# Kernel optimization log

Measured on AMD Instinct MI355X. Metric: run time of the kernel, lower is better.

## Reference

```python
import jax, jax.numpy as jnp
import numpy as np

D_MODEL = 2048
D_INNER = 4096   # expand * d_model == ngroups * d_state
D_XB = 1024
N_HEADS = 32     # = ngroups
HEAD_DIM = 128   # = d_state
N_KV_HEADS = D_XB // HEAD_DIM  # 8
N_REP = N_HEADS // N_KV_HEADS  # 4
D_IN_PROJ = D_INNER + 2 * D_XB + D_INNER + N_HEADS  # 10272
ROPE_BASE = 10000.0


def setup_inputs() -> dict:
    key = jax.random.key(0)
    k1, k2, k3 = jax.random.split(key, 3)
    u = jax.random.normal(k1, (2, 2048, D_MODEL), dtype=jnp.float32)
    W_in = jax.random.normal(k2, (D_IN_PROJ, D_MODEL), dtype=jnp.float32) * (1.0 / np.sqrt(D_MODEL))
    W_out = jax.random.normal(k3, (D_MODEL, D_INNER), dtype=jnp.float32) * (1.0 / np.sqrt(D_INNER))
    return {"u": u, "W_in": W_in, "W_out": W_out}


def _rotate_half(x):
    x1, x2 = jnp.split(x, 2, axis=-1)
    return jnp.concatenate((-x2, x1), axis=-1)


def _rope_cos_sin(seqlen, dim, dtype):
    inv_freq = 1.0 / (ROPE_BASE ** (jnp.arange(0, dim, 2, dtype=jnp.float32) / dim))
    pos = jnp.arange(seqlen, dtype=jnp.float32)
    freqs = pos[:, None] * inv_freq[None, :]          # [S, dim/2]
    emb = jnp.concatenate((freqs, freqs), axis=-1)    # [S, dim]
    return jnp.cos(emb).astype(dtype), jnp.sin(emb).astype(dtype)


def reference(u, W_in, W_out):
    # NOTE: the module's forward short-circuits (early return) into a GQA
    # attention path; the SSM code after the return is dead.
    B, S, _ = u.shape
    zxbcdt = jnp.einsum('bsd,ed->bse', u, W_in)       # [B, S, D_IN_PROJ]
    # split: z (d_inner), x (d_xb), B (d_xb), C (d_inner), dt (nheads); d_mlp = 0
    o0 = D_INNER
    x = zxbcdt[..., o0:o0 + D_XB]
    Bm = zxbcdt[..., o0 + D_XB:o0 + 2 * D_XB]
    C = zxbcdt[..., o0 + 2 * D_XB:o0 + 2 * D_XB + D_INNER]
    # q = C (32 heads), k = B (8 heads), v = x (8 heads); [B, H, S, Dh]
    q = C.reshape(B, S, N_HEADS, HEAD_DIM).transpose(0, 2, 1, 3)
    k = Bm.reshape(B, S, N_KV_HEADS, HEAD_DIM).transpose(0, 2, 1, 3)
    v = x.reshape(B, S, N_KV_HEADS, HEAD_DIM).transpose(0, 2, 1, 3)
    cos, sin = _rope_cos_sin(S, HEAD_DIM, u.dtype)    # [S, Dh]
    cos = cos[None, None]                             # [1, 1, S, Dh]
    sin = sin[None, None]
    q = q * cos + _rotate_half(q) * sin
    k = k * cos + _rotate_half(k) * sin
    # repeat_kv: repeat_interleave along head dim
    k = jnp.repeat(k, N_REP, axis=1)
    v = jnp.repeat(v, N_REP, axis=1)
    scale = 1.0 / np.sqrt(HEAD_DIM)
    scores = jnp.einsum('bhqd,bhkd->bhqk', q, k) * scale
    causal = jnp.tril(jnp.ones((S, S), dtype=bool))
    scores = jnp.where(causal[None, None], scores, jnp.finfo(scores.dtype).min)
    attn = jax.nn.softmax(scores, axis=-1)
    out = jnp.einsum('bhqk,bhkd->bhqd', attn, v)      # [B, H, S, Dh]
    out = out.transpose(0, 2, 1, 3).reshape(B, S, D_INNER)
    return jnp.einsum('bse,de->bsd', out, W_out)      # [B, S, d_model]
```

## Files before the change

### kernel.cpp

```cpp
#include <hip/hip_runtime.h>
#include <stdint.h>

#define S_LEN 2048
#define BATCH 2
#define NH 32
#define NKV 8
#define HD 128
#define NE 6144

typedef __attribute__((ext_vector_type(8))) short short8;
typedef __attribute__((ext_vector_type(4))) float floatx4;

__device__ __forceinline__ unsigned short f2bf(float f) {
    union { float f; uint32_t u; } v; v.f = f;
    uint32_t u = v.u;
    u += 0x7FFFu + ((u >> 16) & 1u);
    return (unsigned short)(u >> 16);
}
__device__ __forceinline__ float bf2f(unsigned short h) {
    union { uint32_t u; float f; } v; v.u = ((uint32_t)h) << 16;
    return v.f;
}
__device__ __forceinline__ uint32_t cvt_pk_bf16(float lo, float hi) {
    uint32_t r;
    asm("v_cvt_pk_bf16_f32 %0, %1, %2" : "=v"(r) : "v"(lo), "v"(hi));
    return r;
}

__global__ void cast_f32_bf16(const float* __restrict__ in,
                              unsigned short* __restrict__ out, int n4) {
    int i = blockIdx.x * blockDim.x + threadIdx.x;
    if (i >= n4) return;
    float4 f = reinterpret_cast<const float4*>(in)[i];
    ushort4 o;
    o.x = f2bf(f.x); o.y = f2bf(f.y); o.z = f2bf(f.z); o.w = f2bf(f.w);
    reinterpret_cast<ushort4*>(out)[i] = o;
}

__device__ __forceinline__ short8 ldfragg(const unsigned short* base, int row, int k8) {
    const int c8 = k8 ^ (row & 7);
    return *reinterpret_cast<const short8*>(base + row * 64 + c8 * 8);
}

template <int OUT_BF16>
__global__ void __launch_bounds__(512, 2)
gemm_256x128(const unsigned short* __restrict__ A, const unsigned short* __restrict__ Bt,
             void* __restrict__ Cv, int M, int N, int K) {
    __shared__ unsigned short As[3][256 * 64];
    __shared__ unsigned short Bs[3][128 * 64];
    const int tid  = threadIdx.x;
    const int w    = tid >> 6;
    const int lane = tid & 63;
    const int quad = lane >> 4;
    const int l16  = lane & 15;
    const int wm   = w >> 1, wn = w & 1;

    const int nwg = gridDim.x * gridDim.y;
    const int cpx = nwg >> 3;
    const int lin = blockIdx.y * gridDim.x + blockIdx.x;
    const int swz = (lin & 7) * cpx + (lin >> 3);
    const int ntx = N >> 7;
    const int m0 = (swz / ntx) << 8;
    const int n0 = (swz % ntx) << 7;

    floatx4 acc[4][4];
#pragma unroll
    for (int i = 0; i < 4; i++)
#pragma unroll
        for (int j = 0; j < 4; j++) acc[i][j] = {0.f, 0.f, 0.f, 0.f};

    const int l8  = lane >> 3;
    const int c8s = (lane & 7) ^ ((lane >> 3) & 7);
    const unsigned short* apA = A  + (size_t)(m0 + w * 32 + l8) * K + c8s * 8;
    const unsigned short* apB = Bt + (size_t)(n0 + w * 16 + l8) * K + c8s * 8;

#define GLD(src, dst) __builtin_amdgcn_global_load_lds(                        \
    (const __attribute__((address_space(1))) void*)(src),                      \
    (__attribute__((address_space(3))) void*)(dst), 16, 0, 0)

#define STG1(bufi, t) do {                     \
    unsigned short* d = &As[bufi][w * 32 * 64];                                \
    const unsigned short* s = apA + (size_t)(t) * 64;                          \
    GLD(s,                   d);                                               \
    GLD(s + (size_t)8  * K,  d + 8  * 64);                                     \
    GLD(s + (size_t)16 * K,  d + 16 * 64);                                     \
} while (0)

#define STG2(bufi, t) do {              \
    unsigned short* dA = &As[bufi][w * 32 * 64];                               \
    const unsigned short* sA = apA + (size_t)(t) * 64;                         \
    GLD(sA + (size_t)24 * K, dA + 24 * 64);                                    \
    unsigned short* dB = &Bs[bufi][w * 16 * 64];                               \
    const unsigned short* sB = apB + (size_t)(t) * 64;                         \
    GLD(sB,                  dB);                                              \
    GLD(sB + (size_t)8 * K,  dB + 8 * 64);                                     \
} while (0)

    STG1(0, 0); STG2(0, 0);
    STG1(1, 1); STG2(1, 1);

    const int NT = K >> 6;
    int bufc = 0;

#pragma unroll 1
    for (int t = 0; t < NT; ++t) {
        const unsigned short* Ab = &As[bufc][0];
        const unsigned short* Bb = &Bs[bufc][0];
        const int bufn = (bufc + 2 >= 3) ? bufc - 1 : bufc + 2;

        if (t < NT - 1) { asm volatile("s_waitcnt vmcnt(6)" ::: "memory"); }
        else            { asm volatile("s_waitcnt vmcnt(0)" ::: "memory"); }
        __builtin_amdgcn_s_barrier();
        asm volatile("" ::: "memory");

        short8 a0[4], b0[4];
#pragma unroll
        for (int mi = 0; mi < 4; ++mi)
            a0[mi] = ldfragg(Ab, wm * 64 + mi * 16 + l16, quad);
#pragma unroll
        for (int ni = 0; ni < 4; ++ni)
            b0[ni] = ldfragg(Bb, wn * 64 + ni * 16 + l16, quad);
        if (t + 2 < NT) { STG1(bufn, t + 2); }
        asm volatile("" ::: "memory");
        __builtin_amdgcn_s_barrier();
        __builtin_amdgcn_s_setprio(1);
#pragma unroll
        for (int mi = 0; mi < 4; ++mi)
#pragma unroll
            for (int ni = 0; ni < 4; ++ni)
                acc[mi][ni] = __builtin_amdgcn_mfma_f32_16x16x32_bf16(a0[mi], b0[ni], acc[mi][ni], 0, 0, 0);
        __builtin_amdgcn_s_setprio(0);
        asm volatile("" ::: "memory");
        __builtin_amdgcn_s_barrier();

        short8 a1[4], b1[4];
#pragma unroll
        for (int mi = 0; mi < 4; ++mi)
            a1[mi] = ldfragg(Ab, wm * 64 + mi * 16 + l16, 4 + quad);
#pragma unroll
        for (int ni = 0; ni < 4; ++ni)
            b1[ni] = ldfragg(Bb, wn * 64 + ni * 16 + l16, 4 + quad);
        if (t + 2 < NT) { STG2(bufn, t + 2); }
        asm volatile("" ::: "memory");
        __builtin_amdgcn_s_barrier();
        __builtin_amdgcn_s_setprio(1);
#pragma unroll
        for (int mi = 0; mi < 4; ++mi)
#pragma unroll
            for (int ni = 0; ni < 4; ++ni)
                acc[mi][ni] = __builtin_amdgcn_mfma_f32_16x16x32_bf16(a1[mi], b1[ni], acc[mi][ni], 0, 0, 0);
        __builtin_amdgcn_s_setprio(0);

        bufc = (bufc + 1 >= 3) ? 0 : bufc + 1;
    }
#undef STG1
#undef STG2
#undef GLD

#pragma unroll
    for (int mi = 0; mi < 4; ++mi)
#pragma unroll
        for (int ni = 0; ni < 4; ++ni) {
            const int row = m0 + wm * 64 + mi * 16 + quad * 4;
            const int col = n0 + wn * 64 + ni * 16 + l16;
#pragma unroll
            for (int r = 0; r < 4; ++r) {
                float vv = acc[mi][ni][r];
                if (OUT_BF16)
                    ((unsigned short*)Cv)[(size_t)(row + r) * N + col] = f2bf(vv);
                else
                    ((float*)Cv)[(size_t)(row + r) * N + col] = vv;
            }
        }
}

#define QSCALE 0.12748539509360f
__global__ void rope_split(const unsigned short* __restrict__ Z,
                           unsigned short* __restrict__ Q,
                           unsigned short* __restrict__ Kb,
                           unsigned short* __restrict__ Vt) {
    const int PER_TOK = 2048 + 512 + 1024;
    int idx = blockIdx.x * blockDim.x + threadIdx.x;
    if (idx >= BATCH * S_LEN * PER_TOK) return;
    int t = idx / PER_TOK;
    int r = idx - t * PER_TOK;
    int b = t / S_LEN, s = t - b * S_LEN;
    const unsigned short* z = Z + (size_t)t * NE;
    if (r < 2048) {
        int h = r >> 6, j = r & 63;
        float x0 = bf2f(z[2048 + h * 128 + j]);
        float x1 = bf2f(z[2048 + h * 128 + j + 64]);
        float inv = exp2f((float)j * -0.20762050593f);
        float c, sn; sincosf((float)s * inv, &sn, &c);
        size_t base = ((size_t)(b * NH + h) * S_LEN + s) * HD;
        Q[base + j]      = f2bf((x0 * c - x1 * sn) * QSCALE);
        Q[base + j + 64] = f2bf((x1 * c + x0 * sn) * QSCALE);
    } else if (r < 2560) {
        int rr = r - 2048; int kh = rr >> 6, j = rr & 63;
        float x0 = bf2f(z[1024 + kh * 128 + j]);
        float x1 = bf2f(z[1024 + kh * 128 + j + 64]);
        float inv = exp2f((float)j * -0.20762050593f);
        float c, sn; sincosf((float)s * inv, &sn, &c);
        size_t base = ((size_t)(b * NKV + kh) * S_LEN + s) * HD;
        Kb[base + j]      = f2bf(x0 * c - x1 * sn);
        Kb[base + j + 64] = f2bf(x1 * c + x0 * sn);
    } else {
        int m = r - 2560; int kh = m >> 7, d = m & 127;
        int k = s & 63;
        int kp = (k & 32) + ((k & 15) << 1) + ((k >> 4) & 1);
        int sp = (s & ~63) | kp;
        Vt[((size_t)(b * NKV + kh) * HD + d) * S_LEN + sp] = z[m];
    }
}

template <bool DIAG>
__device__ __forceinline__ void attn_tile(
    const short8 (&qf)[4], floatx4 (&oacc)[8], float (&lsum)[4],
    const unsigned short* __restrict__ Ks, const unsigned short* __restrict__ Vs,
    unsigned short* __restrict__ pw, int w, int quad, int l16) {
    const int e = l16 & 7;

    floatx4 sacc[4];
#pragma unroll
    for (int nb = 0; nb < 4; nb++) sacc[nb] = {0.f, 0.f, 0.f, 0.f};
    __builtin_amdgcn_s_setprio(1);
#pragma unroll
    for (int ks = 0; ks < 4; ++ks) {
#pragma unroll
        for (int nb = 0; nb < 4; ++nb) {
            const int srow = nb * 16 + l16;
            const int pc = (ks * 4 + quad) ^ e;
            short8 kf = *reinterpret_cast<const short8*>(Ks + srow * 128 + pc * 8);
            sacc[nb] = __builtin_amdgcn_mfma_f32_16x16x32_bf16(qf[ks], kf, sacc[nb], 0, 0, 0);
        }
    }
    __builtin_amdgcn_s_setprio(0);

    float pv[4][4];
#pragma unroll
    for (int nb = 0; nb < 4; ++nb)
#pragma unroll
        for (int r = 0; r < 4; ++r) {
            float p = exp2f(sacc[nb][r]);
            if (DIAG)
                p = (nb * 16 + l16 <= w * 16 + quad * 4 + r) ? p : 0.0f;
            pv[nb][r] = p;
            lsum[r] += p;
        }

    const int row0 = quad * 4;
    const int sub = l16 >> 2, off = (l16 & 3) * 2;
#pragma unroll
    for (int r = 0; r < 4; ++r) {
        const int rowe = (row0 + r) & 7;
#pragma unroll
        for (int g = 0; g < 2; ++g) {
            uint32_t pk = cvt_pk_bf16(pv[g * 2][r], pv[g * 2 + 1][r]);
            const int chunk = (g * 4 + sub) ^ rowe;
            *reinterpret_cast<uint32_t*>(pw + (row0 + r) * 64 + chunk * 8 + off) = pk;
        }
    }

    __builtin_amdgcn_s_setprio(1);
#pragma unroll
    for (int kv_sub = 0; kv_sub < 2; ++kv_sub) {
        const int pcP = (kv_sub * 4 + quad) ^ e;
        short8 pf = *reinterpret_cast<const short8*>(pw + l16 * 64 + pcP * 8);
#pragma unroll
        for (int dt = 0; dt < 8; ++dt) {
            const int drow = dt * 16 + l16;
            const int pcV = (kv_sub * 4 + quad) ^ e;
            short8 vf = *reinterpret_cast<const short8*>(Vs + drow * 64 + pcV * 8);
            oacc[dt] = __builtin_amdgcn_mfma_f32_16x16x32_bf16(pf, vf, oacc[dt], 0, 0, 0);
        }
    }
    __builtin_amdgcn_s_setprio(0);
}

__global__ void __launch_bounds__(256, 4)
attn_kernel(const unsigned short* __restrict__ Q,
            const unsigned short* __restrict__ Kb,
            const unsigned short* __restrict__ Vt,
            unsigned short* __restrict__ Ob) {
    __shared__ unsigned short Ks[64 * 128];
    __shared__ unsigned short Vs[128 * 64];
    __shared__ unsigned short Ps[4][16 * 64];
    const int tid  = threadIdx.x;
    const int w    = tid >> 6;
    const int lane = tid & 63;
    const int quad = lane >> 4;
    const int l16  = lane & 15;
    const int blk = blockIdx.x;
    const int qt = 31 - (blk >> 6);
    const int bh = blk & 63;
    const int h = bh & 31, b = bh >> 5;
    const int kvh = h >> 2;
    const int qw0 = qt * 64 + w * 16;

    const unsigned short* Qbase = Q  + ((size_t)(b * NH  + h)   * S_LEN) * HD;
    const unsigned short* Kbase = Kb + ((size_t)(b * NKV + kvh) * S_LEN) * HD;
    const unsigned short* Vbase = Vt + ((size_t)(b * NKV + kvh) * HD) * S_LEN;

    short8 qf[4];
    {
        const unsigned short* qrow = Qbase + (size_t)(qw0 + l16) * HD + quad * 8;
#pragma unroll
        for (int ks = 0; ks < 4; ++ks)
            qf[ks] = *reinterpret_cast<const short8*>(qrow + ks * 32);
    }

    floatx4 oacc[8];
#pragma unroll
    for (int i = 0; i < 8; i++) oacc[i] = {0.f, 0.f, 0.f, 0.f};
    float lsum[4] = {0.f, 0.f, 0.f, 0.f};

    const unsigned short* kp[4];
    const unsigned short* vp[4];
#pragma unroll
    for (int c = 0; c < 4; ++c) {
        const int bI = w * 4 + c;
        const int krow = bI * 4 + (lane >> 4);
        kp[c] = Kbase + (size_t)krow * HD + ((lane & 15) ^ (krow & 7)) * 8;
        const int drow = bI * 8 + (lane >> 3);
        vp[c] = Vbase + (size_t)drow * S_LEN + ((lane & 7) ^ (drow & 7)) * 8;
    }

#define STAGE() do {                                                           \
    _Pragma("unroll")                                                          \
    for (int c = 0; c < 4; ++c) {                                              \
        const int bI = w * 4 + c;                                              \
        __builtin_amdgcn_global_load_lds(                                      \
            (const __attribute__((address_space(1))) void*)kp[c],              \
            (__attribute__((address_space(3))) void*)(Ks + bI * 512), 16, 0, 0);\
        __builtin_amdgcn_global_load_lds(                                      \
            (const __attribute__((address_space(1))) void*)vp[c],              \
            (__attribute__((address_space(3))) void*)(Vs + bI * 512), 16, 0, 0);\
        kp[c] += 64 * HD; vp[c] += 64;                                         \
    }                                                                          \
} while (0)

    unsigned short* pw = &Ps[w][0];

    for (int t = 0; t < qt; ++t) {
        __syncthreads();
        STAGE();
        __syncthreads();
        attn_tile<false>(qf, oacc, lsum, Ks, Vs, pw, w, quad, l16);
    }
    __syncthreads();
    STAGE();
    __syncthreads();
    attn_tile<true>(qf, oacc, lsum, Ks, Vs, pw, w, quad, l16);
#undef STAGE

    float linv[4];
#pragma unroll
    for (int r = 0; r < 4; ++r) {
        float s = lsum[r];
#pragma unroll
        for (int off = 1; off < 16; off <<= 1) s += __shfl_xor(s, off);
        linv[r] = 1.0f / s;
    }
#pragma unroll
    for (int dt = 0; dt < 8; ++dt) {
        const int d = dt * 16 + l16;
#pragma unroll
        for (int r = 0; r < 4; ++r) {
            const int row = qw0 + quad * 4 + r;
            Ob[((size_t)(b * S_LEN + row)) * 4096 + h * 128 + d] = f2bf(oacc[dt][r] * linv[r]);
        }
    }
}

extern "C" void kernel_launch(void* const* d_in, const int* in_sizes, int n_in,
                              void* d_out, int out_size, void* d_ws, size_t ws_size,
                              hipStream_t stream) {
    const float* u     = (const float*)d_in[0];
    const float* W_in  = (const float*)d_in[1];
    const float* W_out = (const float*)d_in[2];
    float* out = (float*)d_out;

    char* ws = (char*)d_ws;
    unsigned short* u_bf    = (unsigned short*)(ws);
    unsigned short* win_bf  = (unsigned short*)(ws + 16777216);
    unsigned short* wout_bf = (unsigned short*)(ws + 41943040);
    unsigned short* Z       = (unsigned short*)(ws + 58720256);
    unsigned short* Qb      = (unsigned short*)(ws + 109051904);
    unsigned short* Kv      = (unsigned short*)(ws + 142606336);
    unsigned short* Vt      = (unsigned short*)(ws + 150994944);
    unsigned short* Ob      = (unsigned short*)(ws + 159383552);

    {
        int n4 = (2 * 2048 * 2048) / 4;
        cast_f32_bf16<<<(n4 + 255) / 256, 256, 0, stream>>>(u, u_bf, n4);
        n4 = (6144 * 2048) / 4;
        cast_f32_bf16<<<(n4 + 255) / 256, 256, 0, stream>>>(W_in + (size_t)4096 * 2048, win_bf, n4);
        n4 = (2048 * 4096) / 4;
        cast_f32_bf16<<<(n4 + 255) / 256, 256, 0, stream>>>(W_out, wout_bf, n4);
    }
    {
        dim3 g(6144 / 128, 4096 / 256);
        gemm_256x128<1><<<g, 512, 0, stream>>>(u_bf, win_bf, Z, 4096, 6144, 2048);
    }
    {
        int n = BATCH * S_LEN * 3584;
        rope_split<<<(n + 255) / 256, 256, 0, stream>>>(Z, Qb, Kv, Vt);
    }
    attn_kernel<<<BATCH * NH * (S_LEN / 64), 256, 0, stream>>>(Qb, Kv, Vt, Ob);
    {
        dim3 g(2048 / 128, 4096 / 256);
        gemm_256x128<0><<<g, 512, 0, stream>>>(Ob, wout_bf, out, 4096, 2048, 4096);
    }
}
```

Before: 494.2 us.

## Restructure GEMM main loop to one barrier per tile and add XCD-aware tile mapping

The GEMM K-loop now issues all six global-to-LDS loads for stage t+2 right after a single barrier, instead of splitting them across two half-stages guarded by three barriers. The triple buffer rotates by pointer, and LDS fragment offsets are computed once before the loop. Workgroups are remapped so each XCD owns a contiguous 2D block of M×N tiles, chosen by new launch parameters, to improve L2 reuse of A and B panels. Fewer barriers should cut synchronisation stalls, at the cost of issuing more memory traffic at once and adding per-shape mapping constants that must match the grid.

```diff
diff --git a/kernel.cpp b/kernel.cpp
--- a/kernel.cpp
+++ b/kernel.cpp
@@ -37,15 +37,11 @@
     reinterpret_cast<ushort4*>(out)[i] = o;
 }
 
-__device__ __forceinline__ short8 ldfragg(const unsigned short* base, int row, int k8) {
-    const int c8 = k8 ^ (row & 7);
-    return *reinterpret_cast<const short8*>(base + row * 64 + c8 * 8);
-}
-
 template <int OUT_BF16>
 __global__ void __launch_bounds__(512, 2)
 gemm_256x128(const unsigned short* __restrict__ A, const unsigned short* __restrict__ Bt,
-             void* __restrict__ Cv, int M, int N, int K) {
+             void* __restrict__ Cv, int M, int N, int K,
+             int mcMask, int mcLog2, int nchxLog2, int NC) {
     __shared__ unsigned short As[3][256 * 64];
     __shared__ unsigned short Bs[3][128 * 64];
     const int tid  = threadIdx.x;
@@ -55,19 +51,30 @@
     const int l16  = lane & 15;
     const int wm   = w >> 1, wn = w & 1;
 
-    const int nwg = gridDim.x * gridDim.y;
-    const int cpx = nwg >> 3;
     const int lin = blockIdx.y * gridDim.x + blockIdx.x;
-    const int swz = (lin & 7) * cpx + (lin >> 3);
-    const int ntx = N >> 7;
-    const int m0 = (swz / ntx) << 8;
-    const int n0 = (swz % ntx) << 7;
+    const int xcd = lin & 7, idx = lin >> 3;
+    const int im  = idx & mcMask, inn = idx >> mcLog2;
+    const int mc  = xcd >> nchxLog2, nc = xcd & ((1 << nchxLog2) - 1);
+    const int m0  = ((mc << mcLog2) | im) << 8;
+    const int n0  = (nc * NC + inn) << 7;
 
     floatx4 acc[4][4];
 #pragma unroll
     for (int i = 0; i < 4; i++)
 #pragma unroll
         for (int j = 0; j < 4; j++) acc[i][j] = {0.f, 0.f, 0.f, 0.f};
+
+    int offA[4], offB[4];
+#pragma unroll
+    for (int mi = 0; mi < 4; ++mi) {
+        const int row = wm * 64 + mi * 16 + l16;
+        offA[mi] = row * 64 + ((quad ^ (row & 7)) * 8);
+    }
+#pragma unroll
+    for (int ni = 0; ni < 4; ++ni) {
+        const int row = wn * 64 + ni * 16 + l16;
+        offB[ni] = row * 64 + ((quad ^ (row & 7)) * 8);
+    }
 
     const int l8  = lane >> 3;
     const int c8s = (lane & 7) ^ ((lane >> 3) & 7);
@@ -78,51 +85,43 @@
     (const __attribute__((address_space(1))) void*)(src),                      \
     (__attribute__((address_space(3))) void*)(dst), 16, 0, 0)
 
-#define STG1(bufi, t) do {                     \
-    unsigned short* d = &As[bufi][w * 32 * 64];                                \
-    const unsigned short* s = apA + (size_t)(t) * 64;                          \
-    GLD(s,                   d);                                               \
-    GLD(s + (size_t)8  * K,  d + 8  * 64);                                     \
-    GLD(s + (size_t)16 * K,  d + 16 * 64);                                     \
+#define STAGE6(Adst, Bdst, t) do {                  \
+    unsigned short* dA = (Adst) + w * 32 * 64;                                 \
+    const unsigned short* sA = apA + (size_t)(t) * 64;                         \
+    GLD(sA,                   dA);                                             \
+    GLD(sA + (size_t)8  * K,  dA + 8  * 64);                                   \
+    GLD(sA + (size_t)16 * K,  dA + 16 * 64);                                   \
+    GLD(sA + (size_t)24 * K,  dA + 24 * 64);                                   \
+    unsigned short* dB = (Bdst) + w * 16 * 64;                                 \
+    const unsigned short* sB = apB + (size_t)(t) * 64;                         \
+    GLD(sB,                   dB);                                             \
+    GLD(sB + (size_t)8 * K,   dB + 8 * 64);                                    \
 } while (0)
 
-#define STG2(bufi, t) do {              \
-    unsigned short* dA = &As[bufi][w * 32 * 64];                               \
-    const unsigned short* sA = apA + (size_t)(t) * 64;                         \
-    GLD(sA + (size_t)24 * K, dA + 24 * 64);                                    \
-    unsigned short* dB = &Bs[bufi][w * 16 * 64];                               \
-    const unsigned short* sB = apB + (size_t)(t) * 64;                         \
-    GLD(sB,                  dB);                                              \
-    GLD(sB + (size_t)8 * K,  dB + 8 * 64);                                     \
-} while (0)
-
-    STG1(0, 0); STG2(0, 0);
-    STG1(1, 1); STG2(1, 1);
+    unsigned short *Acur = &As[0][0], *Anxt = &As[1][0], *Afr = &As[2][0];
+    unsigned short *Bcur = &Bs[0][0], *Bnxt = &Bs[1][0], *Bfr = &Bs[2][0];
+
+    STAGE6(Acur, Bcur, 0);
+    STAGE6(Anxt, Bnxt, 1);
 
     const int NT = K >> 6;
-    int bufc = 0;
 
 #pragma unroll 1
     for (int t = 0; t < NT; ++t) {
-        const unsigned short* Ab = &As[bufc][0];
-        const unsigned short* Bb = &Bs[bufc][0];
-        const int bufn = (bufc + 2 >= 3) ? bufc - 1 : bufc + 2;
-
         if (t < NT - 1) { asm volatile("s_waitcnt vmcnt(6)" ::: "memory"); }
         else            { asm volatile("s_waitcnt vmcnt(0)" ::: "memory"); }
         __builtin_amdgcn_s_barrier();
         asm volatile("" ::: "memory");
 
-        short8 a0[4], b0[4];
+        if (t + 2 < NT) { STAGE6(Afr, Bfr, t + 2); }
+
+        short8 a0[4], b0[4], a1[4], b1[4];
 #pragma unroll
         for (int mi = 0; mi < 4; ++mi)
-            a0[mi] = ldfragg(Ab, wm * 64 + mi * 16 + l16, quad);
+            a0[mi] = *reinterpret_cast<const short8*>(Acur + offA[mi]);
 #pragma unroll
         for (int ni = 0; ni < 4; ++ni)
-            b0[ni] = ldfragg(Bb, wn * 64 + ni * 16 + l16, quad);
-        if (t + 2 < NT) { STG1(bufn, t + 2); }
-        asm volatile("" ::: "memory");
-        __builtin_amdgcn_s_barrier();
+            b0[ni] = *reinterpret_cast<const short8*>(Bcur + offB[ni]);
         __builtin_amdgcn_s_setprio(1);
 #pragma unroll
         for (int mi = 0; mi < 4; ++mi)
@@ -130,19 +129,13 @@
             for (int ni = 0; ni < 4; ++ni)
                 acc[mi][ni] = __builtin_amdgcn_mfma_f32_16x16x32_bf16(a0[mi], b0[ni], acc[mi][ni], 0, 0, 0);
         __builtin_amdgcn_s_setprio(0);
-        asm volatile("" ::: "memory");
-        __builtin_amdgcn_s_barrier();
-
-        short8 a1[4], b1[4];
+
 #pragma unroll
         for (int mi = 0; mi < 4; ++mi)
-            a1[mi] = ldfragg(Ab, wm * 64 + mi * 16 + l16, 4 + quad);
+            a1[mi] = *reinterpret_cast<const short8*>(Acur + (offA[mi] ^ 32));
 #pragma unroll
         for (int ni = 0; ni < 4; ++ni)
-            b1[ni] = ldfragg(Bb, wn * 64 + ni * 16 + l16, 4 + quad);
-        if (t + 2 < NT) { STG2(bufn, t + 2); }
-        asm volatile("" ::: "memory");
-        __builtin_amdgcn_s_barrier();
+            b1[ni] = *reinterpret_cast<const short8*>(Bcur + (offB[ni] ^ 32));
         __builtin_amdgcn_s_setprio(1);
 #pragma unroll
         for (int mi = 0; mi < 4; ++mi)
@@ -151,10 +144,10 @@
                 acc[mi][ni] = __builtin_amdgcn_mfma_f32_16x16x32_bf16(a1[mi], b1[ni], acc[mi][ni], 0, 0, 0);
         __builtin_amdgcn_s_setprio(0);
 
-        bufc = (bufc + 1 >= 3) ? 0 : bufc + 1;
-    }
-#undef STG1
-#undef STG2
+        unsigned short* ta = Acur; Acur = Anxt; Anxt = Afr; Afr = ta;
+        unsigned short* tb = Bcur; Bcur = Bnxt; Bnxt = Bfr; Bfr = tb;
+    }
+#undef STAGE6
 #undef GLD
 
 #pragma unroll
@@ -400,7 +393,8 @@
     }
     {
         dim3 g(6144 / 128, 4096 / 256);
-        gemm_256x128<1><<<g, 512, 0, stream>>>(u_bf, win_bf, Z, 4096, 6144, 2048);
+        gemm_256x128<1><<<g, 512, 0, stream>>>(u_bf, win_bf, Z, 4096, 6144, 2048,
+                                               7, 3, 2, 12);
     }
     {
         int n = BATCH * S_LEN * 3584;
@@ -409,6 +403,7 @@
     attn_kernel<<<BATCH * NH * (S_LEN / 64), 256, 0, stream>>>(Qb, Kv, Vt, Ob);
     {
         dim3 g(2048 / 128, 4096 / 256);
-        gemm_256x128<0><<<g, 512, 0, stream>>>(Ob, wout_bf, out, 4096, 2048, 4096);
-    }
-}
+        gemm_256x128<0><<<g, 512, 0, stream>>>(Ob, wout_bf, out, 4096, 2048, 4096,
+                                               3, 2, 1, 8);
+    }
+}
```

After: 525.0 us. +6.2%, slower.
